# Optimization experiments

Hardware: AMD Instinct MI355X
Metric: run time of the kernel (lower is better)

Reference implementation:

```python
import jax, jax.numpy as jnp
import numpy as np

E, T = 200000, 1500000
H, INT, BE, NR, NS = 128, 64, 8, 6, 7
N_BEFORE, N_AFTER = 1, 2


def _w(key, fan_in, fan_out):
    return jax.random.normal(key, (fan_in, fan_out), dtype=jnp.float32) / np.sqrt(fan_in)


def setup_inputs() -> dict:
    key = jax.random.key(0)
    ks = jax.random.split(key, 24)
    inp = {
        "x": jax.random.normal(ks[0], (E, H), dtype=jnp.float32),
        "rbf": jax.random.uniform(ks[1], (E, NR), dtype=jnp.float32),
        "sbf": jax.random.uniform(ks[2], (T, NS * NR), dtype=jnp.float32),
        "idx_kj": jax.random.randint(ks[3], (T,), 0, E),
        "idx_ji": jax.random.randint(ks[4], (T,), 0, E),
        # basis projections (no bias)
        "W_rbf1": _w(ks[5], NR, BE),
        "W_rbf2": _w(ks[6], BE, H),
        "W_sbf1": _w(ks[7], NS * NR, BE),
        "W_sbf2": _w(ks[8], BE, INT),
        # message transforms
        "W_kj": _w(ks[9], H, H),
        "b_kj": jnp.zeros((H,), dtype=jnp.float32),
        "W_ji": _w(ks[10], H, H),
        "b_ji": jnp.zeros((H,), dtype=jnp.float32),
        "W_down": _w(ks[11], H, INT),
        "W_up": _w(ks[12], INT, H),
        # residual layers before skip: [n, 2, H, H]
        "W_before": jax.random.normal(ks[13], (N_BEFORE, 2, H, H), dtype=jnp.float32) / np.sqrt(H),
        "b_before": jnp.zeros((N_BEFORE, 2, H), dtype=jnp.float32),
        "W_lin": _w(ks[14], H, H),
        "b_lin": jnp.zeros((H,), dtype=jnp.float32),
        "W_after": jax.random.normal(ks[15], (N_AFTER, 2, H, H), dtype=jnp.float32) / np.sqrt(H),
        "b_after": jnp.zeros((N_AFTER, 2, H), dtype=jnp.float32),
    }
    return inp


def reference(x, rbf, sbf, idx_kj, idx_ji, W_rbf1, W_rbf2, W_sbf1, W_sbf2,
              W_kj, b_kj, W_ji, b_ji, W_down, W_up,
              W_before, b_before, W_lin, b_lin, W_after, b_after):
    act = jax.nn.silu  # swish

    x_ji = act(x @ W_ji + b_ji)                       # [E, H]
    x_kj = act(x @ W_kj + b_kj)                       # [E, H]

    rbf_p = (rbf @ W_rbf1) @ W_rbf2                   # [E, H]
    x_kj = x_kj * rbf_p
    x_kj = act(x_kj @ W_down)                         # [E, INT]

    sbf_p = (sbf @ W_sbf1) @ W_sbf2                   # [T, INT]
    m = x_kj[idx_kj] * sbf_p                          # gather -> [T, INT]
    agg = jax.ops.segment_sum(m, idx_ji, num_segments=x.shape[0])  # [E, INT]
    x_kj = act(agg @ W_up)                            # [E, H]

    h = x_ji + x_kj
    for i in range(W_before.shape[0]):
        h = h + act(act(h @ W_before[i, 0] + b_before[i, 0]) @ W_before[i, 1] + b_before[i, 1])
    h = act(h @ W_lin + b_lin) + x
    for i in range(W_after.shape[0]):
        h = h + act(act(h @ W_after[i, 0] + b_after[i, 0]) @ W_after[i, 1] + b_after[i, 1])
    return h
```

## Files before the change

### kernel.cpp

```cpp
#include <hip/hip_runtime.h>

#define EN 200000
#define TN 1500000
#define NCHUNK ((TN + 63) >> 6)
#define SCAN_BLK 512
#define NB ((EN + SCAN_BLK - 1) / SCAN_BLK)

typedef short s16x8 __attribute__((ext_vector_type(8)));
typedef float f32x4 __attribute__((ext_vector_type(4)));

#define WJI   0
#define WKJ   16384
#define WDOWN 32768
#define WUP   40960
#define WB0   49152
#define WB1   65536
#define WLIN  81920
#define WA00  98304
#define WA01  114688
#define WA10  131072
#define WA11  147456
#define WSBFP 163840
#define WP_COUNT 167936

__device__ __forceinline__ unsigned short f2bf(float f) {
    unsigned int r;
    asm("v_cvt_pk_bf16_f32 %0, %1, %1" : "=v"(r) : "v"(f));
    return (unsigned short)r;
}
__device__ __forceinline__ unsigned short f2bf_o(float f) {
    unsigned int b = __float_as_uint(f);
    b += 0x7FFFu + ((b >> 16) & 1u);
    return (unsigned short)(b >> 16);
}
__device__ __forceinline__ float bf2f(unsigned short u) {
    return __uint_as_float(((unsigned int)u) << 16);
}
__device__ __forceinline__ float silu_f(float v) {
    return v * __builtin_amdgcn_rcpf(1.f + __expf(-v));
}

#define MFMA(a, b, c) __builtin_amdgcn_mfma_f32_16x16x32_bf16((a), (b), (c), 0, 0, 0)

__global__ void k_prep1(const float* __restrict__ Wr1, const float* __restrict__ Wr2,
                        const float* __restrict__ Ws1, const float* __restrict__ Ws2,
                        float* __restrict__ wrbfc, float* __restrict__ wsbfc) {
    int idx = blockIdx.x * 256 + threadIdx.x;
    if (idx < 768) {
        int r = idx >> 7, c = idx & 127;
        float s = 0.f;
        #pragma unroll
        for (int m = 0; m < 8; m++) s += Wr1[r * 8 + m] * Wr2[m * 128 + c];
        wrbfc[idx] = s;
    }
    int i2 = idx - 768;
    if (i2 >= 0 && i2 < 2688) {
        int r = i2 >> 6, c = i2 & 63;
        float s = 0.f;
        #pragma unroll
        for (int m = 0; m < 8; m++) s += Ws1[r * 8 + m] * Ws2[m * 64 + c];
        wsbfc[i2] = s;
    }
}

__global__ void k_prep2(const float* __restrict__ Wji, const float* __restrict__ Wkj,
                        const float* __restrict__ Wdown, const float* __restrict__ Wup,
                        const float* __restrict__ Wbef, const float* __restrict__ Wlin,
                        const float* __restrict__ Waft, const float* __restrict__ wsbfc,
                        unsigned short* __restrict__ wp) {
    for (int idx = blockIdx.x * 256 + threadIdx.x; idx < WP_COUNT; idx += gridDim.x * 256) {
        const float* src;
        int off, N;
        bool pad42 = false;
        if (idx < WKJ)        { src = Wji;           off = WJI;   N = 128; }
        else if (idx < WDOWN) { src = Wkj;           off = WKJ;   N = 128; }
        else if (idx < WUP)   { src = Wdown;         off = WDOWN; N = 64;  }
        else if (idx < WB0)   { src = Wup;           off = WUP;   N = 128; }
        else if (idx < WB1)   { src = Wbef;          off = WB0;   N = 128; }
        else if (idx < WLIN)  { src = Wbef + 16384;  off = WB1;   N = 128; }
        else if (idx < WA00)  { src = Wlin;          off = WLIN;  N = 128; }
        else if (idx < WA01)  { src = Waft;          off = WA00;  N = 128; }
        else if (idx < WA10)  { src = Waft + 16384;  off = WA01;  N = 128; }
        else if (idx < WA11)  { src = Waft + 32768;  off = WA10;  N = 128; }
        else if (idx < WSBFP) { src = Waft + 49152;  off = WA11;  N = 128; }
        else                  { src = wsbfc;         off = WSBFP; N = 64; pad42 = true; }
        int li = idx - off;
        int j = li & 7, lane = (li >> 3) & 63, rest = li >> 9;
        int ncb = N >> 4;
        int cb = rest % ncb, ks = rest / ncb;
        int k = ks * 32 + ((lane >> 4) << 3) + j;
        int n = cb * 16 + (lane & 15);
        float v = 0.f;
        if (!pad42 || k < 42) v = src[k * N + n];
        wp[idx] = f2bf(v);
    }
}

__global__ __launch_bounds__(256, 4) void k_edge1(
        const float* __restrict__ x, const float* __restrict__ rbf,
        const float* __restrict__ bkj, const float* __restrict__ bji,
        const unsigned short* __restrict__ wp, const float* __restrict__ wrbfc,
        float* __restrict__ xji, unsigned short* __restrict__ xd) {
    __shared__ unsigned short xa[64 * 136];
    __shared__ unsigned short kjt[64 * 136];
    const int tid = threadIdx.x;
    const int row0 = blockIdx.x * 64;
    {
        const float4* src = (const float4*)(x + (size_t)row0 * 128);
        #pragma unroll
        for (int k = 0; k < 8; k++) {
            int idx = tid + k * 256;
            float4 v = src[idx];
            int flat = idx << 2, r = flat >> 7, c = flat & 127;
            ushort4 u; u.x = f2bf(v.x); u.y = f2bf(v.y); u.z = f2bf(v.z); u.w = f2bf(v.w);
            *(ushort4*)&xa[r * 136 + c] = u;
        }
    }
    #pragma unroll
    for (int k = 0; k < 32; k++) {
        int idx = tid + k * 256;
        int r = idx >> 7, c = idx & 127;
        const float* rb = rbf + (size_t)(row0 + r) * 6;
        float s = rb[0] * wrbfc[c] + rb[1] * wrbfc[128 + c] + rb[2] * wrbfc[256 + c]
                + rb[3] * wrbfc[384 + c] + rb[4] * wrbfc[512 + c] + rb[5] * wrbfc[640 + c];
        kjt[r * 136 + c] = f2bf(s);
    }
    __syncthreads();
    const int w = tid >> 6, l = tid & 63, l15 = l & 15, l4 = l >> 4;
    s16x8 af[4];
    {
        const unsigned short* ab = &xa[(w * 16 + l15) * 136 + l4 * 8];
        #pragma unroll
        for (int ks = 0; ks < 4; ks++) af[ks] = *(const s16x8*)(ab + ks * 32);
    }
    #pragma unroll
    for (int cb = 0; cb < 8; cb++) {
        f32x4 accj = {0.f, 0.f, 0.f, 0.f};
        f32x4 acck = {0.f, 0.f, 0.f, 0.f};
        #pragma unroll
        for (int ks = 0; ks < 4; ks++) {
            s16x8 bfj = *(const s16x8*)(wp + WJI + (((ks << 3) + cb) * 64 + l) * 8);
            s16x8 bfk = *(const s16x8*)(wp + WKJ + (((ks << 3) + cb) * 64 + l) * 8);
            accj = MFMA(af[ks], bfj, accj);
            acck = MFMA(af[ks], bfk, acck);
        }
        int col = (cb << 4) + l15;
        float bvj = bji[col];
        float bvk = bkj[col];
        #pragma unroll
        for (int i = 0; i < 4; i++) {
            int r = w * 16 + l4 * 4 + i;
            xji[(size_t)(row0 + r) * 128 + col] = silu_f(accj[i] + bvj);
            float rp = bf2f(kjt[r * 136 + col]);
            kjt[r * 136 + col] = f2bf(silu_f(acck[i] + bvk) * rp);
        }
    }
    __syncthreads();
    s16x8 ag[4];
    {
        const unsigned short* ab = &kjt[(w * 16 + l15) * 136 + l4 * 8];
        #pragma unroll
        for (int ks = 0; ks < 4; ks++) ag[ks] = *(const s16x8*)(ab + ks * 32);
    }
    #pragma unroll
    for (int cb = 0; cb < 4; cb++) {
        f32x4 acc = {0.f, 0.f, 0.f, 0.f};
        #pragma unroll
        for (int ks = 0; ks < 4; ks++) {
            s16x8 bf = *(const s16x8*)(wp + WDOWN + (((ks << 2) + cb) * 64 + l) * 8);
            acc = MFMA(ag[ks], bf, acc);
        }
        int col = (cb << 4) + l15;
        #pragma unroll
        for (int i = 0; i < 4; i++) {
            int r = w * 16 + l4 * 4 + i;
            xd[(size_t)(row0 + r) * 64 + col] = f2bf(silu_f(acc[i]));
        }
    }
}

__global__ void k_hist(const int* __restrict__ iji, int* __restrict__ cnt) {
    for (int t = blockIdx.x * 256 + threadIdx.x; t < TN; t += gridDim.x * 256)
        atomicAdd(&cnt[iji[t]], 1);
}

__global__ __launch_bounds__(SCAN_BLK) void k_scan1(const int* __restrict__ cnt, int* __restrict__ bsum) {
    __shared__ int s[SCAN_BLK];
    int i = threadIdx.x, gi = blockIdx.x * SCAN_BLK + i;
    s[i] = (gi < EN) ? cnt[gi] : 0;
    __syncthreads();
    for (int d = SCAN_BLK >> 1; d > 0; d >>= 1) {
        if (i < d) s[i] += s[i + d];
        __syncthreads();
    }
    if (i == 0) bsum[blockIdx.x] = s[0];
}

__global__ __launch_bounds__(SCAN_BLK) void k_scan2(const int* __restrict__ bsum, int* __restrict__ bscan) {
    __shared__ int s[SCAN_BLK];
    int i = threadIdx.x;
    int v = (i < NB) ? bsum[i] : 0;
    s[i] = v;
    __syncthreads();
    for (int d = 1; d < SCAN_BLK; d <<= 1) {
        int t = (i >= d) ? s[i - d] : 0;
        __syncthreads();
        s[i] += t;
        __syncthreads();
    }
    if (i < NB) bscan[i] = s[i] - v;
}

__global__ __launch_bounds__(SCAN_BLK) void k_scan3(const int* __restrict__ cnt, const int* __restrict__ bscan,
                                                    int* __restrict__ segoff, int* __restrict__ cursor) {
    __shared__ int s[SCAN_BLK];
    int i = threadIdx.x, gi = blockIdx.x * SCAN_BLK + i;
    int c = (gi < EN) ? cnt[gi] : 0;
    s[i] = c;
    __syncthreads();
    for (int d = 1; d < SCAN_BLK; d <<= 1) {
        int t = (i >= d) ? s[i - d] : 0;
        __syncthreads();
        s[i] += t;
        __syncthreads();
    }
    int off = bscan[blockIdx.x] + s[i] - c;
    if (gi < EN) { segoff[gi] = off; cursor[gi] = off; }
    if (blockIdx.x == 0 && i == 0) segoff[EN] = TN;
}

__global__ void k_rank(const int* __restrict__ iji, int* __restrict__ cursor, int* __restrict__ pos) {
    for (int t = blockIdx.x * 256 + threadIdx.x; t < TN; t += gridDim.x * 256)
        pos[t] = atomicAdd(&cursor[iji[t]], 1);
}

__global__ __launch_bounds__(256) void k_mscat(
        const float* __restrict__ sbf, const int* __restrict__ ikj, const int* __restrict__ pos,
        const unsigned short* __restrict__ wp, const unsigned short* __restrict__ xd,
        unsigned short* __restrict__ msort) {
    __shared__ unsigned short sb[64 * 72];
    const int tid = threadIdx.x;
    const int w = tid >> 6, l = tid & 63, l15 = l & 15, l4 = l >> 4;
    for (int idx = tid; idx < 64 * 72; idx += 256) sb[idx] = 0;
    __syncthreads();
    for (int ch = blockIdx.x; ch < NCHUNK; ch += gridDim.x) {
        const int t0 = ch << 6;
        const int nt = min(64, TN - t0);
        const int tot = nt * 42;
        const float* src = sbf + (size_t)t0 * 42;
        for (int idx = tid; idx < tot; idx += 256) {
            int r = idx / 42, c = idx - r * 42;
            sb[r * 72 + c] = f2bf_o(src[idx]);
        }
        __syncthreads();
        s16x8 afr[2];
        {
            const unsigned short* ab = &sb[(w * 16 + l15) * 72 + l4 * 8];
            afr[0] = *(const s16x8*)ab;
            afr[1] = *(const s16x8*)(ab + 32);
        }
        f32x4 accs[4];
        #pragma unroll
        for (int cb = 0; cb < 4; cb++) {
            f32x4 acc = {0.f, 0.f, 0.f, 0.f};
            acc = MFMA(afr[0], *(const s16x8*)(wp + WSBFP + ((cb) * 64 + l) * 8), acc);
            acc = MFMA(afr[1], *(const s16x8*)(wp + WSBFP + ((4 + cb) * 64 + l) * 8), acc);
            accs[cb] = acc;
        }
        #pragma unroll
        for (int i = 0; i < 4; i++) {
            int r = w * 16 + l4 * 4 + i;
            if (r < nt) {
                int t = t0 + r;
                int a = ikj[t];
                size_t mb = (size_t)pos[t] * 64;
                const unsigned short* xr = xd + (size_t)a * 64;
                #pragma unroll
                for (int cb = 0; cb < 4; cb++) {
                    int col = (cb << 4) + l15;
                    msort[mb + col] = f2bf_o(accs[cb][i] * bf2f(xr[col]));
                }
            }
        }
        __syncthreads();
    }
}

__global__ __launch_bounds__(256) void k_seg(
        const unsigned short* __restrict__ msort, const int* __restrict__ segoff,
        float* __restrict__ agg) {
    int e = blockIdx.x * 4 + (threadIdx.x >> 6);
    if (e >= EN) return;
    int l = threadIdx.x & 63;
    int sub = l >> 5, c2 = l & 31;
    int n0 = segoff[e], n1 = segoff[e + 1];
    float a0 = 0.f, a1 = 0.f;
    for (int p = n0 + sub; p < n1; p += 2) {
        unsigned int u = *(const unsigned int*)(msort + (size_t)p * 64 + c2 * 2);
        a0 += bf2f((unsigned short)(u & 0xFFFF));
        a1 += bf2f((unsigned short)(u >> 16));
    }
    a0 += __shfl_xor(a0, 32, 64);
    a1 += __shfl_xor(a1, 32, 64);
    if (sub == 0) {
        float2 o = {a0, a1};
        *(float2*)(agg + (size_t)e * 64 + c2 * 2) = o;
    }
}

__global__ __launch_bounds__(256) void k_trip(
        const float* __restrict__ sbf, const int* __restrict__ ikj, const int* __restrict__ iji,
        const unsigned short* __restrict__ wp, const unsigned short* __restrict__ xd,
        float* __restrict__ agg) {
    __shared__ unsigned short sb[64 * 72];
    const int tid = threadIdx.x;
    const int w = tid >> 6, l = tid & 63, l15 = l & 15, l4 = l >> 4;
    for (int idx = tid; idx < 64 * 72; idx += 256) sb[idx] = 0;
    __syncthreads();
    for (int ch = blockIdx.x; ch < NCHUNK; ch += gridDim.x) {
        const int t0 = ch << 6;
        const int nt = min(64, TN - t0);
        const int tot = nt * 42;
        const float* src = sbf + (size_t)t0 * 42;
        for (int idx = tid; idx < tot; idx += 256) {
            int r = idx / 42, c = idx - r * 42;
            sb[r * 72 + c] = f2bf_o(src[idx]);
        }
        __syncthreads();
        s16x8 afr[2];
        {
            const unsigned short* ab = &sb[(w * 16 + l15) * 72 + l4 * 8];
            afr[0] = *(const s16x8*)ab;
            afr[1] = *(const s16x8*)(ab + 32);
        }
        #pragma unroll
        for (int cb = 0; cb < 4; cb++) {
            f32x4 acc = {0.f, 0.f, 0.f, 0.f};
            acc = MFMA(afr[0], *(const s16x8*)(wp + WSBFP + ((cb) * 64 + l) * 8), acc);
            acc = MFMA(afr[1], *(const s16x8*)(wp + WSBFP + ((4 + cb) * 64 + l) * 8), acc);
            int col = (cb << 4) + l15;
            #pragma unroll
            for (int i = 0; i < 4; i++) {
                int r = w * 16 + l4 * 4 + i;
                if (r < nt) {
                    int t = t0 + r;
                    int a = ikj[t], g = iji[t];
                    float m = acc[i] * bf2f(xd[(size_t)a * 64 + col]);
                    atomicAdd(&agg[(size_t)g * 64 + col], m);
                }
            }
        }
        __syncthreads();
    }
}

__device__ __forceinline__ void layer_reg(float (*h)[4], unsigned short* s0, unsigned short* s1,
                                          const unsigned short* wp0, const float* b0,
                                          const unsigned short* wp1, const float* b1,
                                          int w, int l, int l15, int l4) {
    #pragma unroll
    for (int cb = 0; cb < 8; cb++) {
        int col = (cb << 4) + l15;
        #pragma unroll
        for (int i = 0; i < 4; i++)
            s0[((w << 4) + (l4 << 2) + i) * 136 + col] = f2bf(h[cb][i]);
    }
    __syncthreads();
    {
        const unsigned short* ab = &s0[((w << 4) + l15) * 136 + (l4 << 3)];
        s16x8 a0 = *(const s16x8*)ab, a1 = *(const s16x8*)(ab + 32);
        s16x8 a2 = *(const s16x8*)(ab + 64), a3 = *(const s16x8*)(ab + 96);
        #pragma unroll
        for (int cb = 0; cb < 8; cb++) {
            f32x4 acc = {0.f, 0.f, 0.f, 0.f};
            acc = MFMA(a0, *(const s16x8*)(wp0 + ((cb) * 64 + l) * 8), acc);
            acc = MFMA(a1, *(const s16x8*)(wp0 + ((8 + cb) * 64 + l) * 8), acc);
            acc = MFMA(a2, *(const s16x8*)(wp0 + ((16 + cb) * 64 + l) * 8), acc);
            acc = MFMA(a3, *(const s16x8*)(wp0 + ((24 + cb) * 64 + l) * 8), acc);
            int col = (cb << 4) + l15;
            float bv = b0[col];
            #pragma unroll
            for (int i = 0; i < 4; i++)
                s1[((w << 4) + (l4 << 2) + i) * 136 + col] = f2bf(silu_f(acc[i] + bv));
        }
    }
    __syncthreads();
    {
        const unsigned short* ab = &s1[((w << 4) + l15) * 136 + (l4 << 3)];
        s16x8 a0 = *(const s16x8*)ab, a1 = *(const s16x8*)(ab + 32);
        s16x8 a2 = *(const s16x8*)(ab + 64), a3 = *(const s16x8*)(ab + 96);
        #pragma unroll
        for (int cb = 0; cb < 8; cb++) {
            f32x4 acc = {0.f, 0.f, 0.f, 0.f};
            acc = MFMA(a0, *(const s16x8*)(wp1 + ((cb) * 64 + l) * 8), acc);
            acc = MFMA(a1, *(const s16x8*)(wp1 + ((8 + cb) * 64 + l) * 8), acc);
            acc = MFMA(a2, *(const s16x8*)(wp1 + ((16 + cb) * 64 + l) * 8), acc);
            acc = MFMA(a3, *(const s16x8*)(wp1 + ((24 + cb) * 64 + l) * 8), acc);
            int col = (cb << 4) + l15;
            float bv = b1[col];
            #pragma unroll
            for (int i = 0; i < 4; i++) h[cb][i] += silu_f(acc[i] + bv);
        }
    }
    __syncthreads();
}

__global__ __launch_bounds__(256, 4) void k_edge2(
        const float* __restrict__ agg, const float* __restrict__ x,
        const unsigned short* __restrict__ wp, const float* __restrict__ bbef,
        const float* __restrict__ blin, const float* __restrict__ baft,
        float* __restrict__ out) {
    __shared__ unsigned short aa[64 * 136];
    __shared__ unsigned short bb[64 * 136];
    const int tid = threadIdx.x;
    const int row0 = blockIdx.x * 64;
    const int w = tid >> 6, l = tid & 63, l15 = l & 15, l4 = l >> 4;
    {
        const float4* src = (const float4*)(agg + (size_t)row0 * 64);
        #pragma unroll
        for (int k = 0; k < 4; k++) {
            int idx = tid + k * 256;
            float4 v = src[idx];
            int flat = idx << 2, r = flat >> 6, c = flat & 63;
            ushort4 u; u.x = f2bf(v.x); u.y = f2bf(v.y); u.z = f2bf(v.z); u.w = f2bf(v.w);
            *(ushort4*)&aa[r * 72 + c] = u;
        }
    }
    float h[8][4];
    #pragma unroll
    for (int cb = 0; cb < 8; cb++) {
        int col = (cb << 4) + l15;
        #pragma unroll
        for (int i = 0; i < 4; i++) {
            int r = (w << 4) + (l4 << 2) + i;
            h[cb][i] = out[(size_t)(row0 + r) * 128 + col];
        }
    }
    __syncthreads();
    {
        const unsigned short* ab = &aa[((w << 4) + l15) * 72 + (l4 << 3)];
        s16x8 a0 = *(const s16x8*)ab, a1 = *(const s16x8*)(ab + 32);
        #pragma unroll
        for (int cb = 0; cb < 8; cb++) {
            f32x4 acc = {0.f, 0.f, 0.f, 0.f};
            acc = MFMA(a0, *(const s16x8*)(wp + WUP + ((cb) * 64 + l) * 8), acc);
            acc = MFMA(a1, *(const s16x8*)(wp + WUP + ((8 + cb) * 64 + l) * 8), acc);
            #pragma unroll
            for (int i = 0; i < 4; i++) h[cb][i] += silu_f(acc[i]);
        }
    }
    __syncthreads();
    layer_reg(h, bb, aa, wp + WB0, bbef, wp + WB1, bbef + 128, w, l, l15, l4);
    #pragma unroll
    for (int cb = 0; cb < 8; cb++) {
        int col = (cb << 4) + l15;
        #pragma unroll
        for (int i = 0; i < 4; i++)
            bb[((w << 4) + (l4 << 2) + i) * 136 + col] = f2bf(h[cb][i]);
    }
    __syncthreads();
    {
        const unsigned short* ab = &bb[((w << 4) + l15) * 136 + (l4 << 3)];
        s16x8 a0 = *(const s16x8*)ab, a1 = *(const s16x8*)(ab + 32);
        s16x8 a2 = *(const s16x8*)(ab + 64), a3 = *(const s16x8*)(ab + 96);
        #pragma unroll
        for (int cb = 0; cb < 8; cb++) {
            f32x4 acc = {0.f, 0.f, 0.f, 0.f};
            acc = MFMA(a0, *(const s16x8*)(wp + WLIN + ((cb) * 64 + l) * 8), acc);
            acc = MFMA(a1, *(const s16x8*)(wp + WLIN + ((8 + cb) * 64 + l) * 8), acc);
            acc = MFMA(a2, *(const s16x8*)(wp + WLIN + ((16 + cb) * 64 + l) * 8), acc);
            acc = MFMA(a3, *(const s16x8*)(wp + WLIN + ((24 + cb) * 64 + l) * 8), acc);
            int col = (cb << 4) + l15;
            float bv = blin[col];
            #pragma unroll
            for (int i = 0; i < 4; i++) {
                int r = (w << 4) + (l4 << 2) + i;
                h[cb][i] = silu_f(acc[i] + bv) + x[(size_t)(row0 + r) * 128 + col];
            }
        }
    }
    __syncthreads();
    layer_reg(h, aa, bb, wp + WA00, baft, wp + WA01, baft + 128, w, l, l15, l4);
    layer_reg(h, aa, bb, wp + WA10, baft + 256, wp + WA11, baft + 384, w, l, l15, l4);
    #pragma unroll
    for (int cb = 0; cb < 8; cb++) {
        int col = (cb << 4) + l15;
        #pragma unroll
        for (int i = 0; i < 4; i++) {
            int r = (w << 4) + (l4 << 2) + i;
            out[(size_t)(row0 + r) * 128 + col] = h[cb][i];
        }
    }
}

extern "C" void kernel_launch(void* const* d_in, const int* in_sizes, int n_in,
                              void* d_out, int out_size, void* d_ws, size_t ws_size,
                              hipStream_t stream) {
    const float* x     = (const float*)d_in[0];
    const float* rbf   = (const float*)d_in[1];
    const float* sbf   = (const float*)d_in[2];
    const int*   ikj   = (const int*)d_in[3];
    const int*   iji   = (const int*)d_in[4];
    const float* Wr1   = (const float*)d_in[5];
    const float* Wr2   = (const float*)d_in[6];
    const float* Ws1   = (const float*)d_in[7];
    const float* Ws2   = (const float*)d_in[8];
    const float* Wkj   = (const float*)d_in[9];
    const float* bkj   = (const float*)d_in[10];
    const float* Wji   = (const float*)d_in[11];
    const float* bji   = (const float*)d_in[12];
    const float* Wdown = (const float*)d_in[13];
    const float* Wup   = (const float*)d_in[14];
    const float* Wbef  = (const float*)d_in[15];
    const float* bbef  = (const float*)d_in[16];
    const float* Wlin  = (const float*)d_in[17];
    const float* blin  = (const float*)d_in[18];
    const float* Waft  = (const float*)d_in[19];
    const float* baft  = (const float*)d_in[20];

    char* ws = (char*)d_ws;
    size_t o = 0;
    auto alloc = [&](size_t bytes) { size_t r = o; o = (o + bytes + 255) & ~(size_t)255; return r; };
    size_t o_agg   = alloc((size_t)EN * 64 * 4);
    size_t o_xd    = alloc((size_t)EN * 64 * 2);
    size_t o_wp    = alloc((size_t)WP_COUNT * 2);
    size_t o_wrbfc = alloc(768 * 4);
    size_t o_wsbfc = alloc(2688 * 4);
    size_t o_cnt   = alloc((size_t)EN * 4);
    size_t o_soff  = alloc((size_t)(EN + 1) * 4);
    size_t o_cur   = alloc((size_t)EN * 4);
    size_t o_bsum  = alloc(SCAN_BLK * 4);
    size_t o_bscan = alloc(SCAN_BLK * 4);
    size_t o_pos   = alloc((size_t)TN * 4);
    size_t o_msort = alloc((size_t)TN * 64 * 2);
    size_t need_sorted = o;

    float* agg          = (float*)(ws + o_agg);
    unsigned short* xd  = (unsigned short*)(ws + o_xd);
    unsigned short* wp  = (unsigned short*)(ws + o_wp);
    float* wrbfc        = (float*)(ws + o_wrbfc);
    float* wsbfc        = (float*)(ws + o_wsbfc);
    int* cnt            = (int*)(ws + o_cnt);
    int* segoff         = (int*)(ws + o_soff);
    int* cursor         = (int*)(ws + o_cur);
    int* bsum           = (int*)(ws + o_bsum);
    int* bscan          = (int*)(ws + o_bscan);
    int* pos            = (int*)(ws + o_pos);
    unsigned short* msort = (unsigned short*)(ws + o_msort);
    float* out          = (float*)d_out;

    k_prep1<<<14, 256, 0, stream>>>(Wr1, Wr2, Ws1, Ws2, wrbfc, wsbfc);
    k_prep2<<<656, 256, 0, stream>>>(Wji, Wkj, Wdown, Wup, Wbef, Wlin, Waft, wsbfc, wp);
    k_edge1<<<EN / 64, 256, 0, stream>>>(x, rbf, bkj, bji, wp, wrbfc, out, xd);

    if (ws_size >= need_sorted) {
        hipMemsetAsync(cnt, 0, (size_t)EN * 4, stream);
        k_hist<<<2048, 256, 0, stream>>>(iji, cnt);
        k_scan1<<<NB, SCAN_BLK, 0, stream>>>(cnt, bsum);
        k_scan2<<<1, SCAN_BLK, 0, stream>>>(bsum, bscan);
        k_scan3<<<NB, SCAN_BLK, 0, stream>>>(cnt, bscan, segoff, cursor);
        k_rank<<<2048, 256, 0, stream>>>(iji, cursor, pos);
        k_mscat<<<4096, 256, 0, stream>>>(sbf, ikj, pos, wp, xd, msort);
        k_seg<<<(EN + 3) / 4, 256, 0, stream>>>(msort, segoff, agg);
    } else {
        hipMemsetAsync(agg, 0, (size_t)EN * 64 * 4, stream);
        k_trip<<<4096, 256, 0, stream>>>(sbf, ikj, iji, wp, xd, agg);
    }

    k_edge2<<<EN / 64, 256, 0, stream>>>(agg, x, wp, bbef, blin, baft, out);
}
```

Measured before the change: 633.6 us.

## Fuse segment reduction into edge MLP kernel and prefetch sbf chunks

Removes the separate k_seg kernel. Each k_edge2f block now sums its 64 edges' sorted messages straight into shared memory before running the residual MLP, so the fp32 agg buffer is never written and read back. k_mscat also prefetches the next chunk's sbf values into registers while the current chunk's MFMA and scatter run, to hide global load latency. The fused reduction uses one wave per row and serial per-row loops, which may reduce parallelism and add imbalance to the MLP kernel. The prefetch adds 11 registers per thread.

```diff
diff --git a/kernel.cpp b/kernel.cpp
--- a/kernel.cpp
+++ b/kernel.cpp
@@ -243,14 +243,28 @@
     const int w = tid >> 6, l = tid & 63, l15 = l & 15, l4 = l >> 4;
     for (int idx = tid; idx < 64 * 72; idx += 256) sb[idx] = 0;
     __syncthreads();
-    for (int ch = blockIdx.x; ch < NCHUNK; ch += gridDim.x) {
+    int ch = blockIdx.x;
+    float pf[11];
+    if (ch < NCHUNK) {
+        const float* src = sbf + (size_t)(ch << 6) * 42;
+        int lim = min(2688, (TN - (ch << 6)) * 42);
+        #pragma unroll
+        for (int k = 0; k < 11; k++) {
+            int idx = tid + (k << 8);
+            pf[k] = (idx < lim) ? src[idx] : 0.f;
+        }
+    }
+    for (; ch < NCHUNK; ch += gridDim.x) {
         const int t0 = ch << 6;
         const int nt = min(64, TN - t0);
         const int tot = nt * 42;
-        const float* src = sbf + (size_t)t0 * 42;
-        for (int idx = tid; idx < tot; idx += 256) {
-            int r = idx / 42, c = idx - r * 42;
-            sb[r * 72 + c] = f2bf_o(src[idx]);
+        #pragma unroll
+        for (int k = 0; k < 11; k++) {
+            int idx = tid + (k << 8);
+            if (idx < tot) {
+                int r = idx / 42, c = idx - r * 42;
+                sb[r * 72 + c] = f2bf_o(pf[k]);
+            }
         }
         __syncthreads();
         s16x8 afr[2];
@@ -266,6 +280,16 @@
             acc = MFMA(afr[0], *(const s16x8*)(wp + WSBFP + ((cb) * 64 + l) * 8), acc);
             acc = MFMA(afr[1], *(const s16x8*)(wp + WSBFP + ((4 + cb) * 64 + l) * 8), acc);
             accs[cb] = acc;
+        }
+        int nch = ch + gridDim.x;
+        if (nch < NCHUNK) {
+            const float* nsrc = sbf + (size_t)(nch << 6) * 42;
+            int nlim = min(2688, (TN - (nch << 6)) * 42);
+            #pragma unroll
+            for (int k = 0; k < 11; k++) {
+                int idx = tid + (k << 8);
+                pf[k] = (idx < nlim) ? nsrc[idx] : 0.f;
+            }
         }
         #pragma unroll
         for (int i = 0; i < 4; i++) {
@@ -283,28 +307,6 @@
             }
         }
         __syncthreads();
-    }
-}
-
-__global__ __launch_bounds__(256) void k_seg(
-        const unsigned short* __restrict__ msort, const int* __restrict__ segoff,
-        float* __restrict__ agg) {
-    int e = blockIdx.x * 4 + (threadIdx.x >> 6);
-    if (e >= EN) return;
-    int l = threadIdx.x & 63;
-    int sub = l >> 5, c2 = l & 31;
-    int n0 = segoff[e], n1 = segoff[e + 1];
-    float a0 = 0.f, a1 = 0.f;
-    for (int p = n0 + sub; p < n1; p += 2) {
-        unsigned int u = *(const unsigned int*)(msort + (size_t)p * 64 + c2 * 2);
-        a0 += bf2f((unsigned short)(u & 0xFFFF));
-        a1 += bf2f((unsigned short)(u >> 16));
-    }
-    a0 += __shfl_xor(a0, 32, 64);
-    a1 += __shfl_xor(a1, 32, 64);
-    if (sub == 0) {
-        float2 o = {a0, a1};
-        *(float2*)(agg + (size_t)e * 64 + c2 * 2) = o;
     }
 }
 
@@ -405,27 +407,11 @@
     __syncthreads();
 }
 
-__global__ __launch_bounds__(256, 4) void k_edge2(
-        const float* __restrict__ agg, const float* __restrict__ x,
-        const unsigned short* __restrict__ wp, const float* __restrict__ bbef,
-        const float* __restrict__ blin, const float* __restrict__ baft,
-        float* __restrict__ out) {
-    __shared__ unsigned short aa[64 * 136];
-    __shared__ unsigned short bb[64 * 136];
-    const int tid = threadIdx.x;
-    const int row0 = blockIdx.x * 64;
+__device__ __forceinline__ void edge2_body(
+        unsigned short* aa, unsigned short* bb, const float* x,
+        const unsigned short* wp, const float* bbef, const float* blin,
+        const float* baft, float* out, int row0, int tid) {
     const int w = tid >> 6, l = tid & 63, l15 = l & 15, l4 = l >> 4;
-    {
-        const float4* src = (const float4*)(agg + (size_t)row0 * 64);
-        #pragma unroll
-        for (int k = 0; k < 4; k++) {
-            int idx = tid + k * 256;
-            float4 v = src[idx];
-            int flat = idx << 2, r = flat >> 6, c = flat & 63;
-            ushort4 u; u.x = f2bf(v.x); u.y = f2bf(v.y); u.z = f2bf(v.z); u.w = f2bf(v.w);
-            *(ushort4*)&aa[r * 72 + c] = u;
-        }
-    }
     float h[8][4];
     #pragma unroll
     for (int cb = 0; cb < 8; cb++) {
@@ -491,6 +477,52 @@
             out[(size_t)(row0 + r) * 128 + col] = h[cb][i];
         }
     }
+}
+
+__global__ __launch_bounds__(256, 4) void k_edge2f(
+        const unsigned short* __restrict__ msort, const int* __restrict__ segoff,
+        const float* __restrict__ x, const unsigned short* __restrict__ wp,
+        const float* __restrict__ bbef, const float* __restrict__ blin,
+        const float* __restrict__ baft, float* __restrict__ out) {
+    __shared__ unsigned short aa[64 * 136];
+    __shared__ unsigned short bb[64 * 136];
+    __shared__ int soff[65];
+    const int tid = threadIdx.x;
+    const int row0 = blockIdx.x * 64;
+    const int w = tid >> 6, l = tid & 63;
+    if (tid < 65) soff[tid] = segoff[row0 + tid];
+    __syncthreads();
+    for (int r = w; r < 64; r += 4) {
+        int n0 = soff[r], n1 = soff[r + 1];
+        float s = 0.f;
+        for (int p = n0; p < n1; p++)
+            s += bf2f(msort[(size_t)p * 64 + l]);
+        aa[r * 72 + l] = f2bf(s);
+    }
+    edge2_body(aa, bb, x, wp, bbef, blin, baft, out, row0, tid);
+}
+
+__global__ __launch_bounds__(256, 4) void k_edge2(
+        const float* __restrict__ agg, const float* __restrict__ x,
+        const unsigned short* __restrict__ wp, const float* __restrict__ bbef,
+        const float* __restrict__ blin, const float* __restrict__ baft,
+        float* __restrict__ out) {
+    __shared__ unsigned short aa[64 * 136];
+    __shared__ unsigned short bb[64 * 136];
+    const int tid = threadIdx.x;
+    const int row0 = blockIdx.x * 64;
+    {
+        const float4* src = (const float4*)(agg + (size_t)row0 * 64);
+        #pragma unroll
+        for (int k = 0; k < 4; k++) {
+            int idx = tid + k * 256;
+            float4 v = src[idx];
+            int flat = idx << 2, r = flat >> 6, c = flat & 63;
+            ushort4 u; u.x = f2bf(v.x); u.y = f2bf(v.y); u.z = f2bf(v.z); u.w = f2bf(v.w);
+            *(ushort4*)&aa[r * 72 + c] = u;
+        }
+    }
+    edge2_body(aa, bb, x, wp, bbef, blin, baft, out, row0, tid);
 }
 
 extern "C" void kernel_launch(void* const* d_in, const int* in_sizes, int n_in,
@@ -561,11 +593,10 @@
         k_scan3<<<NB, SCAN_BLK, 0, stream>>>(cnt, bscan, segoff, cursor);
         k_rank<<<2048, 256, 0, stream>>>(iji, cursor, pos);
         k_mscat<<<4096, 256, 0, stream>>>(sbf, ikj, pos, wp, xd, msort);
-        k_seg<<<(EN + 3) / 4, 256, 0, stream>>>(msort, segoff, agg);
+        k_edge2f<<<EN / 64, 256, 0, stream>>>(msort, segoff, x, wp, bbef, blin, baft, out);
     } else {
         hipMemsetAsync(agg, 0, (size_t)EN * 64 * 4, stream);
         k_trip<<<4096, 256, 0, stream>>>(sbf, ikj, iji, wp, xd, agg);
-    }
-
-    k_edge2<<<EN / 64, 256, 0, stream>>>(agg, x, wp, bbef, blin, baft, out);
-}
+        k_edge2<<<EN / 64, 256, 0, stream>>>(agg, x, wp, bbef, blin, baft, out);
+    }
+}
```

After: 710.2 us. +12.1%, slower.
